# Kernel optimization log

Hardware: AMD Instinct MI355X
Metric: run time of the kernel (lower is better)

Reference implementation:

```python
import jax, jax.numpy as jnp
import numpy as np

EPS = 1e-12  # F.normalize default eps


def _l2norm(x, axis):
    n = jnp.sqrt(jnp.sum(x * x, axis=axis, keepdims=True))
    return x / jnp.maximum(n, EPS)


def setup_inputs() -> dict:
    key = jax.random.key(0)
    k1, k2, k3, k4 = jax.random.split(key, 4)
    N, T, C, K = 64, 577, 768, 64
    return {
        "grids": jax.random.normal(k1, (N, T, C), dtype=jnp.float32),
        "conv_w": jax.random.normal(k2, (K, C), dtype=jnp.float32) * 0.03,
        "conv_b": jax.random.normal(k3, (K,), dtype=jnp.float32) * 0.01,
        "centroids": jax.random.normal(k4, (K, C), dtype=jnp.float32) * 0.03,
    }


def reference(grids, conv_w, conv_b, centroids):
    # grids: (N, 577, 768) -> (N, C=768, T=577), matching view+permute in torch
    N = grids.shape[0]
    x = jnp.transpose(grids.reshape(N, 577, 768), (0, 2, 1))  # (N, C, T)
    # per-token L2 normalization over channel dim
    x = _l2norm(x, axis=1)
    # 1x1 conv == per-token linear: (N, K, T)
    logits = jnp.einsum('kc,nct->nkt', conv_w, x) + conv_b[None, :, None]
    a = jax.nn.softmax(logits, axis=1)  # softmax over regions K
    # NetVLAD algebraic rewrite of sum_t a[n,k,t]*(x[n,:,t]-c[k,:]):
    #   = (a @ x^T)[n,k,c] - sum_t(a)[n,k] * c[k,c]
    p = jnp.einsum('nkt,nct->nkc', a, x) - a.sum(axis=-1)[:, :, None] * centroids[None]
    p = _l2norm(p, axis=2)             # intra-region normalization
    p = p.reshape(N, -1)               # (N, K*C)
    p = _l2norm(p, axis=1)             # global normalization
    return p
```

## Files before the change

### kernel.cpp

```cpp
#include <hip/hip_runtime.h>
#include <hip/hip_bf16.h>
#include <math.h>

#define TT 577
#define TP 640
#define CCH 768
#define KR 64
#define NB 64

typedef __attribute__((ext_vector_type(8))) short bf16x8;
typedef __attribute__((ext_vector_type(8))) unsigned short ushort8;
typedef __attribute__((ext_vector_type(4))) float f32x4;

static constexpr float EPSF = 1e-12f;

static __device__ inline unsigned short f2bf(float f) {
    return __bfloat16_as_ushort(__float2bfloat16(f));
}

__global__ __launch_bounds__(256, 3) void k_logits(
    const float* __restrict__ grids,
    const float* __restrict__ conv_w,
    const float* __restrict__ conv_b,
    unsigned short* __restrict__ ws_a,
    float* __restrict__ ws_asum)
{
    __shared__ __align__(16) unsigned short Wl[2][KR * 136];

    const int tid  = threadIdx.x;
    const int lane = tid & 63;
    const int w    = tid >> 6;
    const int n    = blockIdx.x / 10;
    const int tb   = (blockIdx.x - n * 10) << 6;
    const int t0w  = tb + (w << 4);

    const int lr = lane & 15;
    const int lg = lane >> 4;

    const int tokA = t0w + lr;
    const bool validA = (tokA < TT);
    const float* gsrc = grids + ((size_t)n * TT + tokA) * CCH + (lg << 3);

    float4 wreg[4][2];
    auto load_w = [&](int c0) {
        #pragma unroll
        for (int it = 0; it < 4; ++it) {
            int f = tid + (it << 8);
            int kr = f >> 4, c8 = (f & 15) << 3;
            const float* src = conv_w + (size_t)kr * CCH + c0 + c8;
            wreg[it][0] = *reinterpret_cast<const float4*>(src);
            wreg[it][1] = *reinterpret_cast<const float4*>(src + 4);
        }
    };
    auto store_w = [&](int buf) {
        #pragma unroll
        for (int it = 0; it < 4; ++it) {
            int f = tid + (it << 8);
            int kr = f >> 4, c8 = (f & 15) << 3;
            ushort8 o;
            o[0] = f2bf(wreg[it][0].x); o[1] = f2bf(wreg[it][0].y);
            o[2] = f2bf(wreg[it][0].z); o[3] = f2bf(wreg[it][0].w);
            o[4] = f2bf(wreg[it][1].x); o[5] = f2bf(wreg[it][1].y);
            o[6] = f2bf(wreg[it][1].z); o[7] = f2bf(wreg[it][1].w);
            *reinterpret_cast<ushort8*>(&Wl[buf][kr * 136 + c8]) = o;
        }
    };

    f32x4 acc[4] = {};
    float ss = 0.f;

    load_w(0);
    store_w(0);
    __syncthreads();

    for (int ch = 0; ch < 6; ++ch) {
        if (ch < 5) {
            load_w((ch + 1) << 7);
            store_w((ch + 1) & 1);
        }
        const int c0 = ch << 7;
        const unsigned short* Wb = Wl[ch & 1];

        #pragma unroll
        for (int s = 0; s < 4; ++s) {
            float a8[8];
            if (validA) {
                float4 u0 = *reinterpret_cast<const float4*>(gsrc + c0 + (s << 5));
                float4 u1 = *reinterpret_cast<const float4*>(gsrc + c0 + (s << 5) + 4);
                a8[0]=u0.x; a8[1]=u0.y; a8[2]=u0.z; a8[3]=u0.w;
                a8[4]=u1.x; a8[5]=u1.y; a8[6]=u1.z; a8[7]=u1.w;
            } else {
                #pragma unroll
                for (int j = 0; j < 8; ++j) a8[j] = 0.f;
            }
            bf16x8 afrag;
            #pragma unroll
            for (int j = 0; j < 8; ++j) {
                ss = fmaf(a8[j], a8[j], ss);
                ((unsigned short*)&afrag)[j] = f2bf(a8[j]);
            }
            const int cl = (s << 5) + (lg << 3);
            #pragma unroll
            for (int rt = 0; rt < 4; ++rt) {
                bf16x8 bfrag = *reinterpret_cast<const bf16x8*>(&Wb[(rt*16 + lr)*136 + cl]);
                acc[rt] = __builtin_amdgcn_mfma_f32_16x16x32_bf16(afrag, bfrag, acc[rt], 0, 0, 0);
            }
        }
        __syncthreads();
    }

    ss += __shfl_xor(ss, 16);
    ss += __shfl_xor(ss, 32);
    const float nrm = sqrtf(ss);
    const float inv = 1.0f / fmaxf(nrm, EPSF);

    float b_[4];
    #pragma unroll
    for (int rt = 0; rt < 4; ++rt) b_[rt] = conv_b[rt*16 + lr];

    float invT[4];
    #pragma unroll
    for (int reg = 0; reg < 4; ++reg) invT[reg] = __shfl(inv, (lg << 2) + reg);

    float lgt[4][4], mx[4];
    #pragma unroll
    for (int reg = 0; reg < 4; ++reg) {
        float m = -1e30f;
        #pragma unroll
        for (int rt = 0; rt < 4; ++rt) {
            lgt[rt][reg] = fmaf(acc[rt][reg], invT[reg], b_[rt]);
            m = fmaxf(m, lgt[rt][reg]);
        }
        mx[reg] = m;
    }
    #pragma unroll
    for (int msk = 1; msk < 16; msk <<= 1) {
        #pragma unroll
        for (int reg = 0; reg < 4; ++reg) mx[reg] = fmaxf(mx[reg], __shfl_xor(mx[reg], msk));
    }
    float ex[4][4], sm[4] = {0.f, 0.f, 0.f, 0.f};
    #pragma unroll
    for (int rt = 0; rt < 4; ++rt) {
        #pragma unroll
        for (int reg = 0; reg < 4; ++reg) {
            ex[rt][reg] = __expf(lgt[rt][reg] - mx[reg]);
            sm[reg] += ex[rt][reg];
        }
    }
    #pragma unroll
    for (int msk = 1; msk < 16; msk <<= 1) {
        #pragma unroll
        for (int reg = 0; reg < 4; ++reg) sm[reg] += __shfl_xor(sm[reg], msk);
    }

    float rsm[4];
    #pragma unroll
    for (int reg = 0; reg < 4; ++reg) {
        const bool vt = (t0w + (lg << 2) + reg) < TT;
        rsm[reg] = vt ? (1.0f / sm[reg]) : 0.f;
    }

    float pa[4];
    #pragma unroll
    for (int rt = 0; rt < 4; ++rt) {
        pa[rt] = ex[rt][0]*rsm[0] + ex[rt][1]*rsm[1] + ex[rt][2]*rsm[2] + ex[rt][3]*rsm[3];
        pa[rt] += __shfl_xor(pa[rt], 16);
        pa[rt] += __shfl_xor(pa[rt], 32);
    }
    float* asum_lds = reinterpret_cast<float*>(&Wl[1][0]);
    if (lane < 16) {
        #pragma unroll
        for (int rt = 0; rt < 4; ++rt)
            asum_lds[(w << 6) + rt*16 + lane] = pa[rt];
    }

    unsigned short* Abuf = &Wl[0][0] + (size_t)w * KR * 24;
    #pragma unroll
    for (int reg = 0; reg < 4; ++reg) {
        const int trow = (lg << 2) + reg;
        const float scale = invT[reg] * rsm[reg];
        #pragma unroll
        for (int rt = 0; rt < 4; ++rt)
            Abuf[(rt*16 + lr)*24 + trow] = f2bf(ex[rt][reg] * scale);
    }
    __syncthreads();

    if (tid < 64)
        ws_asum[(size_t)blockIdx.x * 64 + tid] =
            asum_lds[tid] + asum_lds[64 + tid] + asum_lds[128 + tid] + asum_lds[192 + tid];

    {
        ushort8 r0 = *reinterpret_cast<const ushort8*>(&Abuf[lane * 24]);
        ushort8 r1 = *reinterpret_cast<const ushort8*>(&Abuf[lane * 24 + 8]);
        unsigned short* dst = ws_a + ((size_t)n * KR + lane) * TP + t0w;
        *reinterpret_cast<ushort8*>(dst)     = r0;
        *reinterpret_cast<ushort8*>(dst + 8) = r1;
    }
}

#define LOADA(d0,d1,d2,d3,t0_)                                                   \
    d0 = *reinterpret_cast<const bf16x8*>(abase +           (size_t)(t0_));      \
    d1 = *reinterpret_cast<const bf16x8*>(abase + 16*TP +   (size_t)(t0_));      \
    d2 = *reinterpret_cast<const bf16x8*>(abase + 32*TP +   (size_t)(t0_));      \
    d3 = *reinterpret_cast<const bf16x8*>(abase + 48*TP +   (size_t)(t0_));

#define LOADB(d,t0_) do {                                                        \
    const int tb2_ = (t0_) + (lg << 3);                                          \
    if ((t0_) + 32 <= TT) {                                                      \
        _Pragma("unroll")                                                        \
        for (int j_ = 0; j_ < 8; ++j_)                                           \
            ((unsigned short*)&(d))[j_] = f2bf(gb[(size_t)(tb2_ + j_) * CCH]);   \
    } else {                                                                     \
        _Pragma("unroll")                                                        \
        for (int j_ = 0; j_ < 8; ++j_) {                                         \
            float v_ = (tb2_ + j_ < TT) ? gb[(size_t)(tb2_ + j_) * CCH] : 0.f;   \
            ((unsigned short*)&(d))[j_] = f2bf(v_);                              \
        }                                                                        \
    } } while (0)

__global__ __launch_bounds__(256, 4) void k_vlad(
    const float* __restrict__ grids,
    const unsigned short* __restrict__ ws_a,
    const float* __restrict__ ws_asum,
    const float* __restrict__ centroids,
    float* __restrict__ out)
{
    __shared__ float asum_s[64];

    const int tid  = threadIdx.x;
    const int lane = tid & 63;
    const int w    = tid >> 6;
    const int n    = blockIdx.x / 12;
    const int c0   = (blockIdx.x - n * 12) << 6;
    const int lr   = lane & 15;
    const int lg   = lane >> 4;

    if (tid < 64) {
        float s = 0.f;
        #pragma unroll
        for (int b = 0; b < 10; ++b)
            s += ws_asum[((size_t)n * 10 + b) * 64 + tid];
        asum_s[tid] = s;
    }
    __syncthreads();

    const int c = c0 + (w << 4) + lr;
    const unsigned short* abase = ws_a + ((size_t)n * KR + lr) * TP + (lg << 3);
    const float* gb = grids + (size_t)n * TT * CCH + c;

    f32x4 acc0 = {}, acc1 = {}, acc2 = {}, acc3 = {};
    bf16x8 a0, a1, a2, a3, b0;
    bf16x8 p0, p1, p2, p3, q0;

    LOADA(a0, a1, a2, a3, 0)
    LOADB(b0, 0);

    int t0 = 0;
    while (true) {
        int tn = t0 + 32;
        if (tn < TT) { LOADA(p0, p1, p2, p3, tn) LOADB(q0, tn); }
        acc0 = __builtin_amdgcn_mfma_f32_16x16x32_bf16(a0, b0, acc0, 0, 0, 0);
        acc1 = __builtin_amdgcn_mfma_f32_16x16x32_bf16(a1, b0, acc1, 0, 0, 0);
        acc2 = __builtin_amdgcn_mfma_f32_16x16x32_bf16(a2, b0, acc2, 0, 0, 0);
        acc3 = __builtin_amdgcn_mfma_f32_16x16x32_bf16(a3, b0, acc3, 0, 0, 0);
        t0 = tn;
        if (t0 >= TT) break;

        tn = t0 + 32;
        if (tn < TT) { LOADA(a0, a1, a2, a3, tn) LOADB(b0, tn); }
        acc0 = __builtin_amdgcn_mfma_f32_16x16x32_bf16(p0, q0, acc0, 0, 0, 0);
        acc1 = __builtin_amdgcn_mfma_f32_16x16x32_bf16(p1, q0, acc1, 0, 0, 0);
        acc2 = __builtin_amdgcn_mfma_f32_16x16x32_bf16(p2, q0, acc2, 0, 0, 0);
        acc3 = __builtin_amdgcn_mfma_f32_16x16x32_bf16(p3, q0, acc3, 0, 0, 0);
        t0 = tn;
        if (t0 >= TT) break;
    }

    #pragma unroll
    for (int reg = 0; reg < 4; ++reg) {
        {
            const int kr = 0*16 + (lg << 2) + reg;
            out[((size_t)n * KR + kr) * CCH + c] =
                acc0[reg] - asum_s[kr] * centroids[(size_t)kr * CCH + c];
        }
        {
            const int kr = 1*16 + (lg << 2) + reg;
            out[((size_t)n * KR + kr) * CCH + c] =
                acc1[reg] - asum_s[kr] * centroids[(size_t)kr * CCH + c];
        }
        {
            const int kr = 2*16 + (lg << 2) + reg;
            out[((size_t)n * KR + kr) * CCH + c] =
                acc2[reg] - asum_s[kr] * centroids[(size_t)kr * CCH + c];
        }
        {
            const int kr = 3*16 + (lg << 2) + reg;
            out[((size_t)n * KR + kr) * CCH + c] =
                acc3[reg] - asum_s[kr] * centroids[(size_t)kr * CCH + c];
        }
    }
}

__global__ __launch_bounds__(256) void kc_norm_kernel(float* __restrict__ out)
{
    const int tid = threadIdx.x;
    const int sub = tid >> 6;
    const int l   = tid & 63;
    float4* p = reinterpret_cast<float4*>(out) + ((size_t)blockIdx.x * 4 + sub) * 192;
    float4 v0 = p[l];
    float4 v1 = p[l + 64];
    float4 v2 = p[l + 128];
    float ss = v0.x*v0.x + v0.y*v0.y + v0.z*v0.z + v0.w*v0.w
             + v1.x*v1.x + v1.y*v1.y + v1.z*v1.z + v1.w*v1.w
             + v2.x*v2.x + v2.y*v2.y + v2.z*v2.z + v2.w*v2.w;
    #pragma unroll
    for (int m = 1; m < 64; m <<= 1) ss += __shfl_xor(ss, m);
    const float sc = 0.125f / fmaxf(sqrtf(ss), EPSF);
    v0.x*=sc; v0.y*=sc; v0.z*=sc; v0.w*=sc;
    v1.x*=sc; v1.y*=sc; v1.z*=sc; v1.w*=sc;
    v2.x*=sc; v2.y*=sc; v2.z*=sc; v2.w*=sc;
    p[l] = v0;
    p[l + 64] = v1;
    p[l + 128] = v2;
}

extern "C" void kernel_launch(void* const* d_in, const int* in_sizes, int n_in,
                              void* d_out, int out_size, void* d_ws, size_t ws_size,
                              hipStream_t stream)
{
    const float* grids     = (const float*)d_in[0];
    const float* conv_w    = (const float*)d_in[1];
    const float* conv_b    = (const float*)d_in[2];
    const float* centroids = (const float*)d_in[3];
    float* out = (float*)d_out;

    unsigned short* ws_a    = (unsigned short*)d_ws;
    float*          ws_asum = (float*)((char*)d_ws + 5242880);

    hipLaunchKernelGGL(k_logits, dim3(NB * 10), dim3(256), 0, stream,
                       grids, conv_w, conv_b, ws_a, ws_asum);
    hipLaunchKernelGGL(k_vlad, dim3(NB * 12), dim3(256), 0, stream,
                       grids, ws_a, ws_asum, centroids, out);
    hipLaunchKernelGGL(kc_norm_kernel, dim3(NB * KR / 4), dim3(256), 0, stream, out);
}
```

Measured before the change: 71.86 us.

## Preconvert conv weights to bf16 and run logits with one-wave blocks

A new prep kernel converts conv_w to bf16 once and zeroes the padded tail of the attention workspace. The logits kernel then uses 64-thread blocks of 16 tokens, giving 37 token blocks per batch item. Each wave reads the bf16 weights straight from global memory into registers with software double-buffering, which removes the LDS staging and per-chunk barriers. Partial a-sums are written per block and reduced over 37 entries in the vlad kernel. This adds a kernel launch and redundant weight reads through the cache.

```diff
diff --git a/kernel.cpp b/kernel.cpp
--- a/kernel.cpp
+++ b/kernel.cpp
@@ -4,6 +4,7 @@
 
 #define TT 577
 #define TP 640
+#define TBL 37
 #define CCH 768
 #define KR 64
 #define NB 64
@@ -18,21 +19,78 @@
     return __bfloat16_as_ushort(__float2bfloat16(f));
 }
 
-__global__ __launch_bounds__(256, 3) void k_logits(
+__global__ __launch_bounds__(256) void k_prep(
+    const float* __restrict__ conv_w,
+    unsigned short* __restrict__ ws_w,
+    unsigned short* __restrict__ ws_a)
+{
+    const int g = blockIdx.x * 256 + threadIdx.x;
+    if (g < 6144) {
+        const float* s = conv_w + (size_t)g * 8;
+        float4 v0 = *reinterpret_cast<const float4*>(s);
+        float4 v1 = *reinterpret_cast<const float4*>(s + 4);
+        ushort8 o;
+        o[0]=f2bf(v0.x); o[1]=f2bf(v0.y); o[2]=f2bf(v0.z); o[3]=f2bf(v0.w);
+        o[4]=f2bf(v1.x); o[5]=f2bf(v1.y); o[6]=f2bf(v1.z); o[7]=f2bf(v1.w);
+        *reinterpret_cast<ushort8*>(ws_w + (size_t)g * 8) = o;
+    }
+    if (g < 4096) {
+        unsigned short* d = ws_a + (size_t)g * TP + 592;
+        ushort8 z = {0,0,0,0,0,0,0,0};
+        #pragma unroll
+        for (int i = 0; i < 6; ++i)
+            *reinterpret_cast<ushort8*>(d + i * 8) = z;
+    }
+}
+
+#define LG2(u0_,u1_, cc_)                                                      \
+    if (validA) {                                                              \
+        u0_ = *reinterpret_cast<const float4*>(gsrc + (cc_));                  \
+        u1_ = *reinterpret_cast<const float4*>(gsrc + (cc_) + 4);              \
+    } else {                                                                   \
+        u0_ = make_float4(0.f,0.f,0.f,0.f);                                    \
+        u1_ = make_float4(0.f,0.f,0.f,0.f);                                    \
+    }
+
+#define LW2(b0_,b1_,b2_,b3_, cc_)                                              \
+    b0_ = *reinterpret_cast<const bf16x8*>(wbase +            (cc_));          \
+    b1_ = *reinterpret_cast<const bf16x8*>(wbase + 16*CCH +   (cc_));          \
+    b2_ = *reinterpret_cast<const bf16x8*>(wbase + 32*CCH +   (cc_));          \
+    b3_ = *reinterpret_cast<const bf16x8*>(wbase + 48*CCH +   (cc_));
+
+#define STEP2(u0_,u1_, b0_,b1_,b2_,b3_)                                        \
+    {                                                                          \
+        ss = fmaf(u0_.x,u0_.x, fmaf(u0_.y,u0_.y, fmaf(u0_.z,u0_.z,             \
+             fmaf(u0_.w,u0_.w, fmaf(u1_.x,u1_.x, fmaf(u1_.y,u1_.y,             \
+             fmaf(u1_.z,u1_.z, fmaf(u1_.w,u1_.w, ss))))))));                   \
+        bf16x8 afrag;                                                          \
+        ((unsigned short*)&afrag)[0] = f2bf(u0_.x);                            \
+        ((unsigned short*)&afrag)[1] = f2bf(u0_.y);                            \
+        ((unsigned short*)&afrag)[2] = f2bf(u0_.z);                            \
+        ((unsigned short*)&afrag)[3] = f2bf(u0_.w);                            \
+        ((unsigned short*)&afrag)[4] = f2bf(u1_.x);                            \
+        ((unsigned short*)&afrag)[5] = f2bf(u1_.y);                            \
+        ((unsigned short*)&afrag)[6] = f2bf(u1_.z);                            \
+        ((unsigned short*)&afrag)[7] = f2bf(u1_.w);                            \
+        acc[0] = __builtin_amdgcn_mfma_f32_16x16x32_bf16(afrag, b0_, acc[0], 0, 0, 0); \
+        acc[1] = __builtin_amdgcn_mfma_f32_16x16x32_bf16(afrag, b1_, acc[1], 0, 0, 0); \
+        acc[2] = __builtin_amdgcn_mfma_f32_16x16x32_bf16(afrag, b2_, acc[2], 0, 0, 0); \
+        acc[3] = __builtin_amdgcn_mfma_f32_16x16x32_bf16(afrag, b3_, acc[3], 0, 0, 0); \
+    }
+
+__global__ __launch_bounds__(64, 4) void k_logits(
     const float* __restrict__ grids,
-    const float* __restrict__ conv_w,
+    const unsigned short* __restrict__ ws_w,
     const float* __restrict__ conv_b,
     unsigned short* __restrict__ ws_a,
     float* __restrict__ ws_asum)
 {
-    __shared__ __align__(16) unsigned short Wl[2][KR * 136];
-
-    const int tid  = threadIdx.x;
-    const int lane = tid & 63;
-    const int w    = tid >> 6;
-    const int n    = blockIdx.x / 10;
-    const int tb   = (blockIdx.x - n * 10) << 6;
-    const int t0w  = tb + (w << 4);
+    __shared__ __align__(16) unsigned short Abuf[KR * 24];
+
+    const int lane = threadIdx.x;
+    const int n    = blockIdx.x / TBL;
+    const int tbi  = blockIdx.x - n * TBL;
+    const int t0w  = tbi << 4;
 
     const int lr = lane & 15;
     const int lg = lane >> 4;
@@ -40,73 +98,27 @@
     const int tokA = t0w + lr;
     const bool validA = (tokA < TT);
     const float* gsrc = grids + ((size_t)n * TT + tokA) * CCH + (lg << 3);
-
-    float4 wreg[4][2];
-    auto load_w = [&](int c0) {
-        #pragma unroll
-        for (int it = 0; it < 4; ++it) {
-            int f = tid + (it << 8);
-            int kr = f >> 4, c8 = (f & 15) << 3;
-            const float* src = conv_w + (size_t)kr * CCH + c0 + c8;
-            wreg[it][0] = *reinterpret_cast<const float4*>(src);
-            wreg[it][1] = *reinterpret_cast<const float4*>(src + 4);
-        }
-    };
-    auto store_w = [&](int buf) {
-        #pragma unroll
-        for (int it = 0; it < 4; ++it) {
-            int f = tid + (it << 8);
-            int kr = f >> 4, c8 = (f & 15) << 3;
-            ushort8 o;
-            o[0] = f2bf(wreg[it][0].x); o[1] = f2bf(wreg[it][0].y);
-            o[2] = f2bf(wreg[it][0].z); o[3] = f2bf(wreg[it][0].w);
-            o[4] = f2bf(wreg[it][1].x); o[5] = f2bf(wreg[it][1].y);
-            o[6] = f2bf(wreg[it][1].z); o[7] = f2bf(wreg[it][1].w);
-            *reinterpret_cast<ushort8*>(&Wl[buf][kr * 136 + c8]) = o;
-        }
-    };
+    const unsigned short* wbase = ws_w + (size_t)lr * CCH + (lg << 3);
 
     f32x4 acc[4] = {};
     float ss = 0.f;
 
-    load_w(0);
-    store_w(0);
-    __syncthreads();
-
-    for (int ch = 0; ch < 6; ++ch) {
-        if (ch < 5) {
-            load_w((ch + 1) << 7);
-            store_w((ch + 1) & 1);
-        }
-        const int c0 = ch << 7;
-        const unsigned short* Wb = Wl[ch & 1];
-
-        #pragma unroll
-        for (int s = 0; s < 4; ++s) {
-            float a8[8];
-            if (validA) {
-                float4 u0 = *reinterpret_cast<const float4*>(gsrc + c0 + (s << 5));
-                float4 u1 = *reinterpret_cast<const float4*>(gsrc + c0 + (s << 5) + 4);
-                a8[0]=u0.x; a8[1]=u0.y; a8[2]=u0.z; a8[3]=u0.w;
-                a8[4]=u1.x; a8[5]=u1.y; a8[6]=u1.z; a8[7]=u1.w;
-            } else {
-                #pragma unroll
-                for (int j = 0; j < 8; ++j) a8[j] = 0.f;
-            }
-            bf16x8 afrag;
-            #pragma unroll
-            for (int j = 0; j < 8; ++j) {
-                ss = fmaf(a8[j], a8[j], ss);
-                ((unsigned short*)&afrag)[j] = f2bf(a8[j]);
-            }
-            const int cl = (s << 5) + (lg << 3);
-            #pragma unroll
-            for (int rt = 0; rt < 4; ++rt) {
-                bf16x8 bfrag = *reinterpret_cast<const bf16x8*>(&Wb[(rt*16 + lr)*136 + cl]);
-                acc[rt] = __builtin_amdgcn_mfma_f32_16x16x32_bf16(afrag, bfrag, acc[rt], 0, 0, 0);
-            }
-        }
-        __syncthreads();
+    float4 xa0, xa1, xb0, xb1;
+    bf16x8 wa0, wa1, wa2, wa3, wb0, wb1, wb2, wb3;
+
+    LG2(xa0, xa1, 0)
+    LW2(wa0, wa1, wa2, wa3, 0)
+    #pragma unroll
+    for (int cp = 0; cp < 12; ++cp) {
+        const int cc = cp << 6;
+        LG2(xb0, xb1, cc + 32)
+        LW2(wb0, wb1, wb2, wb3, cc + 32)
+        STEP2(xa0, xa1, wa0, wa1, wa2, wa3)
+        if (cp < 11) {
+            LG2(xa0, xa1, cc + 64)
+            LW2(wa0, wa1, wa2, wa3, cc + 64)
+        }
+        STEP2(xb0, xb1, wb0, wb1, wb2, wb3)
     }
 
     ss += __shfl_xor(ss, 16);
@@ -167,14 +179,12 @@
         pa[rt] += __shfl_xor(pa[rt], 16);
         pa[rt] += __shfl_xor(pa[rt], 32);
     }
-    float* asum_lds = reinterpret_cast<float*>(&Wl[1][0]);
     if (lane < 16) {
         #pragma unroll
         for (int rt = 0; rt < 4; ++rt)
-            asum_lds[(w << 6) + rt*16 + lane] = pa[rt];
-    }
-
-    unsigned short* Abuf = &Wl[0][0] + (size_t)w * KR * 24;
+            ws_asum[((size_t)n * TBL + tbi) * 64 + rt*16 + lane] = pa[rt];
+    }
+
     #pragma unroll
     for (int reg = 0; reg < 4; ++reg) {
         const int trow = (lg << 2) + reg;
@@ -184,10 +194,6 @@
             Abuf[(rt*16 + lr)*24 + trow] = f2bf(ex[rt][reg] * scale);
     }
     __syncthreads();
-
-    if (tid < 64)
-        ws_asum[(size_t)blockIdx.x * 64 + tid] =
-            asum_lds[tid] + asum_lds[64 + tid] + asum_lds[128 + tid] + asum_lds[192 + tid];
 
     {
         ushort8 r0 = *reinterpret_cast<const ushort8*>(&Abuf[lane * 24]);
@@ -237,9 +243,8 @@
 
     if (tid < 64) {
         float s = 0.f;
-        #pragma unroll
-        for (int b = 0; b < 10; ++b)
-            s += ws_asum[((size_t)n * 10 + b) * 64 + tid];
+        for (int b = 0; b < TBL; ++b)
+            s += ws_asum[((size_t)n * TBL + b) * 64 + tid];
         asum_s[tid] = s;
     }
     __syncthreads();
@@ -336,9 +341,12 @@
 
     unsigned short* ws_a    = (unsigned short*)d_ws;
     float*          ws_asum = (float*)((char*)d_ws + 5242880);
-
-    hipLaunchKernelGGL(k_logits, dim3(NB * 10), dim3(256), 0, stream,
-                       grids, conv_w, conv_b, ws_a, ws_asum);
+    unsigned short* ws_w    = (unsigned short*)((char*)d_ws + 5849088);
+
+    hipLaunchKernelGGL(k_prep, dim3(64), dim3(256), 0, stream,
+                       conv_w, ws_w, ws_a);
+    hipLaunchKernelGGL(k_logits, dim3(NB * TBL), dim3(64), 0, stream,
+                       grids, ws_w, conv_b, ws_a, ws_asum);
     hipLaunchKernelGGL(k_vlad, dim3(NB * 12), dim3(256), 0, stream,
                        grids, ws_a, ws_asum, centroids, out);
     hipLaunchKernelGGL(kc_norm_kernel, dim3(NB * KR / 4), dim3(256), 0, stream, out);
```

New measurement: 137.6 us. 91.4% more time.

## Stage grid tiles through double-buffered LDS in logits kernel with coalesced loads

Applied to the files above, without the earlier changes.

The logits kernel now loads grid tiles cooperatively with coalesced float4 reads, converts them to bf16 into a double-buffered LDS tile, and overlaps the next chunk's global loads with the current MFMA steps. Previously each lane read its own token row straight from global memory. The sum of squares for normalization is now computed from the bf16-rounded values, which slightly changes precision. A small prep kernel zeroes the padded tail columns of the attention workspace, and occupancy drops to two blocks per CU because of the larger LDS footprint.

```diff
diff --git a/kernel.cpp b/kernel.cpp
--- a/kernel.cpp
+++ b/kernel.cpp
@@ -7,6 +7,7 @@
 #define CCH 768
 #define KR 64
 #define NB 64
+#define LSTR 136
 
 typedef __attribute__((ext_vector_type(8))) short bf16x8;
 typedef __attribute__((ext_vector_type(8))) unsigned short ushort8;
@@ -17,15 +18,111 @@
 static __device__ inline unsigned short f2bf(float f) {
     return __bfloat16_as_ushort(__float2bfloat16(f));
 }
-
-__global__ __launch_bounds__(256, 3) void k_logits(
+static __device__ inline float bf2f(unsigned short b) {
+    union { unsigned int u; float f; } v; v.u = ((unsigned int)b) << 16;
+    return v.f;
+}
+
+__global__ __launch_bounds__(256) void k_prep(unsigned short* __restrict__ ws_a)
+{
+    const int g = blockIdx.x * 256 + threadIdx.x;
+    unsigned short* d = ws_a + (size_t)g * TP + 592;
+    ushort8 z = {0,0,0,0,0,0,0,0};
+    #pragma unroll
+    for (int i = 0; i < 6; ++i)
+        *reinterpret_cast<ushort8*>(d + i * 8) = z;
+}
+
+
+#define STAGE_G(c0_)                                                           \
+    {                                                                          \
+        _Pragma("unroll")                                                      \
+        for (int it = 0; it < 4; ++it) {                                       \
+            const int u  = (it << 8) + tid;                                    \
+            const int tk = u >> 4, sl = u & 15;                                \
+            if (tb + tk < TT) {                                                \
+                const float* s_ = grids + ((size_t)n * TT + tb + tk) * CCH     \
+                                  + (c0_) + (sl << 3);                         \
+                gr[it][0] = *reinterpret_cast<const float4*>(s_);              \
+                gr[it][1] = *reinterpret_cast<const float4*>(s_ + 4);          \
+            } else {                                                           \
+                gr[it][0] = make_float4(0.f,0.f,0.f,0.f);                      \
+                gr[it][1] = make_float4(0.f,0.f,0.f,0.f);                      \
+            }                                                                  \
+        }                                                                      \
+    }
+
+#define STAGE_W(c0_)                                                           \
+    {                                                                          \
+        _Pragma("unroll")                                                      \
+        for (int it = 0; it < 4; ++it) {                                       \
+            const int u  = (it << 8) + tid;                                    \
+            const int kr = u >> 4, sl = u & 15;                                \
+            const float* s_ = conv_w + (size_t)kr * CCH + (c0_) + (sl << 3);   \
+            wr[it][0] = *reinterpret_cast<const float4*>(s_);                  \
+            wr[it][1] = *reinterpret_cast<const float4*>(s_ + 4);              \
+        }                                                                      \
+    }
+
+#define CVT8(dst_, a_, b_)                                                     \
+    { dst_[0]=f2bf(a_.x); dst_[1]=f2bf(a_.y); dst_[2]=f2bf(a_.z);              \
+      dst_[3]=f2bf(a_.w); dst_[4]=f2bf(b_.x); dst_[5]=f2bf(b_.y);              \
+      dst_[6]=f2bf(b_.z); dst_[7]=f2bf(b_.w); }
+
+#define WRITE_G(buf_)                                                          \
+    {                                                                          \
+        _Pragma("unroll")                                                      \
+        for (int it = 0; it < 4; ++it) {                                       \
+            const int u  = (it << 8) + tid;                                    \
+            const int tk = u >> 4, sl = u & 15;                                \
+            ushort8 o;                                                         \
+            CVT8(o, gr[it][0], gr[it][1])                                      \
+            *reinterpret_cast<ushort8*>(&Gs[buf_][tk * LSTR + (sl << 3)]) = o; \
+        }                                                                      \
+    }
+
+#define WRITE_W(buf_)                                                          \
+    {                                                                          \
+        _Pragma("unroll")                                                      \
+        for (int it = 0; it < 4; ++it) {                                       \
+            const int u  = (it << 8) + tid;                                    \
+            const int kr = u >> 4, sl = u & 15;                                \
+            ushort8 o;                                                         \
+            CVT8(o, wr[it][0], wr[it][1])                                      \
+            *reinterpret_cast<ushort8*>(&Ws[buf_][kr * LSTR + (sl << 3)]) = o; \
+        }                                                                      \
+    }
+
+#define KSTEP(buf_, s_)                                                        \
+    {                                                                          \
+        bf16x8 af = *reinterpret_cast<const bf16x8*>(                          \
+            &Gs[buf_][((w << 4) + lr) * LSTR + ((((s_) << 2) + lg) << 3)]);    \
+        _Pragma("unroll")                                                      \
+        for (int j = 0; j < 8; ++j) {                                          \
+            const float v_ = bf2f(((unsigned short*)&af)[j]);                  \
+            ss = fmaf(v_, v_, ss);                                             \
+        }                                                                      \
+        const int csl = (((s_) << 2) + lg) << 3;                               \
+        bf16x8 b0_ = *reinterpret_cast<const bf16x8*>(&Ws[buf_][ lr       * LSTR + csl]); \
+        bf16x8 b1_ = *reinterpret_cast<const bf16x8*>(&Ws[buf_][(16 + lr) * LSTR + csl]); \
+        bf16x8 b2_ = *reinterpret_cast<const bf16x8*>(&Ws[buf_][(32 + lr) * LSTR + csl]); \
+        bf16x8 b3_ = *reinterpret_cast<const bf16x8*>(&Ws[buf_][(48 + lr) * LSTR + csl]); \
+        acc[0] = __builtin_amdgcn_mfma_f32_16x16x32_bf16(af, b0_, acc[0], 0, 0, 0); \
+        acc[1] = __builtin_amdgcn_mfma_f32_16x16x32_bf16(af, b1_, acc[1], 0, 0, 0); \
+        acc[2] = __builtin_amdgcn_mfma_f32_16x16x32_bf16(af, b2_, acc[2], 0, 0, 0); \
+        acc[3] = __builtin_amdgcn_mfma_f32_16x16x32_bf16(af, b3_, acc[3], 0, 0, 0); \
+    }
+
+__global__ __launch_bounds__(256, 2) void k_logits(
     const float* __restrict__ grids,
     const float* __restrict__ conv_w,
     const float* __restrict__ conv_b,
     unsigned short* __restrict__ ws_a,
     float* __restrict__ ws_asum)
 {
-    __shared__ __align__(16) unsigned short Wl[2][KR * 136];
+    __shared__ __align__(16) unsigned short Gs[2][64 * LSTR];
+    __shared__ __align__(16) unsigned short Ws[2][64 * LSTR];
+    __shared__ float asum_lds[4][64];
 
     const int tid  = threadIdx.x;
     const int lane = tid & 63;
@@ -37,75 +134,20 @@
     const int lr = lane & 15;
     const int lg = lane >> 4;
 
-    const int tokA = t0w + lr;
-    const bool validA = (tokA < TT);
-    const float* gsrc = grids + ((size_t)n * TT + tokA) * CCH + (lg << 3);
-
-    float4 wreg[4][2];
-    auto load_w = [&](int c0) {
-        #pragma unroll
-        for (int it = 0; it < 4; ++it) {
-            int f = tid + (it << 8);
-            int kr = f >> 4, c8 = (f & 15) << 3;
-            const float* src = conv_w + (size_t)kr * CCH + c0 + c8;
-            wreg[it][0] = *reinterpret_cast<const float4*>(src);
-            wreg[it][1] = *reinterpret_cast<const float4*>(src + 4);
-        }
-    };
-    auto store_w = [&](int buf) {
-        #pragma unroll
-        for (int it = 0; it < 4; ++it) {
-            int f = tid + (it << 8);
-            int kr = f >> 4, c8 = (f & 15) << 3;
-            ushort8 o;
-            o[0] = f2bf(wreg[it][0].x); o[1] = f2bf(wreg[it][0].y);
-            o[2] = f2bf(wreg[it][0].z); o[3] = f2bf(wreg[it][0].w);
-            o[4] = f2bf(wreg[it][1].x); o[5] = f2bf(wreg[it][1].y);
-            o[6] = f2bf(wreg[it][1].z); o[7] = f2bf(wreg[it][1].w);
-            *reinterpret_cast<ushort8*>(&Wl[buf][kr * 136 + c8]) = o;
-        }
-    };
-
+    float4 gr[4][2], wr[4][2];
     f32x4 acc[4] = {};
     float ss = 0.f;
 
-    load_w(0);
-    store_w(0);
+    STAGE_G(0) STAGE_W(0)
+    WRITE_G(0) WRITE_W(0)
     __syncthreads();
 
+    #pragma unroll
     for (int ch = 0; ch < 6; ++ch) {
-        if (ch < 5) {
-            load_w((ch + 1) << 7);
-            store_w((ch + 1) & 1);
-        }
-        const int c0 = ch << 7;
-        const unsigned short* Wb = Wl[ch & 1];
-
-        #pragma unroll
-        for (int s = 0; s < 4; ++s) {
-            float a8[8];
-            if (validA) {
-                float4 u0 = *reinterpret_cast<const float4*>(gsrc + c0 + (s << 5));
-                float4 u1 = *reinterpret_cast<const float4*>(gsrc + c0 + (s << 5) + 4);
-                a8[0]=u0.x; a8[1]=u0.y; a8[2]=u0.z; a8[3]=u0.w;
-                a8[4]=u1.x; a8[5]=u1.y; a8[6]=u1.z; a8[7]=u1.w;
-            } else {
-                #pragma unroll
-                for (int j = 0; j < 8; ++j) a8[j] = 0.f;
-            }
-            bf16x8 afrag;
-            #pragma unroll
-            for (int j = 0; j < 8; ++j) {
-                ss = fmaf(a8[j], a8[j], ss);
-                ((unsigned short*)&afrag)[j] = f2bf(a8[j]);
-            }
-            const int cl = (s << 5) + (lg << 3);
-            #pragma unroll
-            for (int rt = 0; rt < 4; ++rt) {
-                bf16x8 bfrag = *reinterpret_cast<const bf16x8*>(&Wb[(rt*16 + lr)*136 + cl]);
-                acc[rt] = __builtin_amdgcn_mfma_f32_16x16x32_bf16(afrag, bfrag, acc[rt], 0, 0, 0);
-            }
-        }
+        const int buf = ch & 1;
+        if (ch < 5) { STAGE_G((ch + 1) << 7) STAGE_W((ch + 1) << 7) }
+        KSTEP(buf, 0) KSTEP(buf, 1) KSTEP(buf, 2) KSTEP(buf, 3)
+        if (ch < 5) { WRITE_G(buf ^ 1) WRITE_W(buf ^ 1) }
         __syncthreads();
     }
 
@@ -167,14 +209,13 @@
         pa[rt] += __shfl_xor(pa[rt], 16);
         pa[rt] += __shfl_xor(pa[rt], 32);
     }
-    float* asum_lds = reinterpret_cast<float*>(&Wl[1][0]);
     if (lane < 16) {
         #pragma unroll
         for (int rt = 0; rt < 4; ++rt)
-            asum_lds[(w << 6) + rt*16 + lane] = pa[rt];
-    }
-
-    unsigned short* Abuf = &Wl[0][0] + (size_t)w * KR * 24;
+            asum_lds[w][rt*16 + lane] = pa[rt];
+    }
+
+    unsigned short* Abuf = &Gs[0][0] + (size_t)w * KR * 24;
     #pragma unroll
     for (int reg = 0; reg < 4; ++reg) {
         const int trow = (lg << 2) + reg;
@@ -187,7 +228,7 @@
 
     if (tid < 64)
         ws_asum[(size_t)blockIdx.x * 64 + tid] =
-            asum_lds[tid] + asum_lds[64 + tid] + asum_lds[128 + tid] + asum_lds[192 + tid];
+            asum_lds[0][tid] + asum_lds[1][tid] + asum_lds[2][tid] + asum_lds[3][tid];
 
     {
         ushort8 r0 = *reinterpret_cast<const ushort8*>(&Abuf[lane * 24]);
@@ -337,6 +378,7 @@
     unsigned short* ws_a    = (unsigned short*)d_ws;
     float*          ws_asum = (float*)((char*)d_ws + 5242880);
 
+    hipLaunchKernelGGL(k_prep, dim3(16), dim3(256), 0, stream, ws_a);
     hipLaunchKernelGGL(k_logits, dim3(NB * 10), dim3(256), 0, stream,
                        grids, conv_w, conv_b, ws_a, ws_asum);
     hipLaunchKernelGGL(k_vlad, dim3(NB * 12), dim3(256), 0, stream,
```

Result: slower. 85.23 us (+18.6%).
